# Performance work log

Measured on AMD Instinct MI355X. Metric: run time of the kernel, lower is better.

The kernel has to match this reference:

```python
import jax, jax.numpy as jnp
import numpy as np


def setup_inputs() -> dict:
    key = jax.random.key(0)
    k1, k2 = jax.random.split(key)
    n, d, ic, oc, r = 128, 256, 16, 16, 10
    x = jax.random.normal(k1, (n, d, ic, r), dtype=jnp.float32)
    weights = jax.random.normal(k2, (d, ic, oc, r), dtype=jnp.float32)
    return {"x": x, "weights": weights}


def reference(x, weights):
    # x: [n, d, ic, r]; weights: [d, ic, oc, r]
    # log_softmax over in_channels (dim=1 of weights)
    log_weights = jax.nn.log_softmax(weights, axis=1)  # [d, ic, oc, r]
    # broadcast add: x[n,d,ic,1,r] + lw[d,ic,oc,r] -> [n,d,ic,oc,r]
    z = x[:, :, :, None, :] + log_weights[None]
    # logsumexp over ic -> [n, d, oc, r]
    return jax.nn.logsumexp(z, axis=2)
```

## Files before the change

### kernel.cpp

```cpp
#include <hip/hip_runtime.h>
#include <hip/hip_bf16.h>


typedef __attribute__((ext_vector_type(8))) short bf16x8;
typedef __attribute__((ext_vector_type(4))) float f32x4;

__device__ __forceinline__ unsigned short f2bf(float v) {
    unsigned u = __float_as_uint(v);
    u += 0x7FFF + ((u >> 16) & 1);
    return (unsigned short)(u >> 16);
}

__global__ __launch_bounds__(256, 2) void fused_mfma_kernel(const float* __restrict__ x,
                                                            const float* __restrict__ w,
                                                            float* __restrict__ out) {
    __shared__ __align__(16) unsigned short es[64 * 328];
    __shared__ __align__(16) unsigned short ws_[10 * 640];
    __shared__ float lcs[160];

    const int tid = threadIdx.x;
    const int d   = blockIdx.x & 255;
    const int nb  = (blockIdx.x >> 8) << 6;

    {
        const int n_l = tid >> 2;
        const int seg = tid & 3;
        const float* xg = x + ((nb + n_l) * 256 + d) * 160 + seg * 40;
        float4 xv[10];
#pragma unroll
        for (int k = 0; k < 10; ++k) xv[k] = *reinterpret_cast<const float4*>(xg + 4 * k);

        const float* wgp = w + d * 2560 + tid * 10;
        float wv[10];
#pragma unroll
        for (int k = 0; k < 5; ++k) {
            float2 v = *reinterpret_cast<const float2*>(wgp + 2 * k);
            wv[2 * k] = v.x; wv[2 * k + 1] = v.y;
        }

        const float* xf = reinterpret_cast<const float*>(xv);
#pragma unroll
        for (int r = 0; r < 10; ++r) {
            unsigned short s0 = f2bf(__expf(xf[r]));
            unsigned short s1 = f2bf(__expf(xf[10 + r]));
            unsigned short s2 = f2bf(__expf(xf[20 + r]));
            unsigned short s3 = f2bf(__expf(xf[30 + r]));
            const unsigned lo = (unsigned)s0 | ((unsigned)s1 << 16);
            const unsigned hi = (unsigned)s2 | ((unsigned)s3 << 16);
            unsigned* dst = reinterpret_cast<unsigned*>(&es[n_l * 328 + r * 32 + 4 * seg]);
            *reinterpret_cast<uint2*>(dst) = make_uint2(lo, hi);
            unsigned* pad = reinterpret_cast<unsigned*>(&es[n_l * 328 + r * 32 + 16 + 4 * seg]);
            *reinterpret_cast<uint2*>(pad) = make_uint2(0u, 0u);
        }
#pragma unroll
        for (int k = 0; k < 10; ++k) {
            const int off = tid * 10 + k;
            const int ic  = off / 160;
            const int rem = off - ic * 160;
            const int oc  = rem / 10;
            const int r   = rem - oc * 10;
            ws_[r * 640 + oc * 40 + ic] = f2bf(__expf(wv[k]));
        }
        if (tid < 160) {
            const int r = tid >> 4, oc = tid & 15;
            uint4* p = reinterpret_cast<uint4*>(&ws_[r * 640 + oc * 40 + 16]);
            const uint4 z = make_uint4(0u, 0u, 0u, 0u);
            p[0] = z; p[1] = z;
        }
    }
    __syncthreads();

    if (tid < 160) {
        const int oc = tid / 10, r = tid - (tid / 10) * 10;
        const unsigned short* p = &ws_[r * 640 + oc * 40];
        float s = 0.f;
#pragma unroll
        for (int ic = 0; ic < 16; ++ic)
            s += __uint_as_float(((unsigned)p[ic]) << 16);
        lcs[oc * 10 + r] = __logf(s);
    }

    const int mt = tid >> 6;
    const int l  = tid & 63;
    const int lm = l & 15;
    const int kg = l >> 4;

    const int abase = (mt * 16 + lm) * 328 + kg * 8;
    const int bbase = lm * 40 + kg * 8;

    f32x4 acc[10];
    const f32x4 zero = {0.f, 0.f, 0.f, 0.f};
#pragma unroll
    for (int r = 0; r < 10; ++r) {
        bf16x8 a = *reinterpret_cast<const bf16x8*>(&es[abase + r * 32]);
        bf16x8 b = *reinterpret_cast<const bf16x8*>(&ws_[r * 640 + bbase]);
        acc[r] = __builtin_amdgcn_mfma_f32_16x16x32_bf16(a, b, zero, 0, 0, 0);
    }
    __syncthreads();

    float lc[10];
#pragma unroll
    for (int r = 0; r < 10; ++r) lc[r] = lcs[lm * 10 + r];

#pragma unroll
    for (int j = 0; j < 4; ++j) {
        const int n = mt * 16 + kg * 4 + j;
        float* og = out + ((nb + n) * 256 + d) * 160 + lm * 10;
#pragma unroll
        for (int h = 0; h < 5; ++h) {
            float2 o;
            o.x = __logf(acc[2 * h][j])     - lc[2 * h];
            o.y = __logf(acc[2 * h + 1][j]) - lc[2 * h + 1];
            *reinterpret_cast<float2*>(og + 2 * h) = o;
        }
    }
}

extern "C" void kernel_launch(void* const* d_in, const int* in_sizes, int n_in,
                              void* d_out, int out_size, void* d_ws, size_t ws_size,
                              hipStream_t stream) {
    const float* x = (const float*)d_in[0];
    const float* w = (const float*)d_in[1];
    float* out = (float*)d_out;

    fused_mfma_kernel<<<512, 256, 0, stream>>>(x, w, out);
}
```

Measured before the change: 16.52 us.

## Halve batch tile per block and split r across waves to double grid

```diff
diff --git a/kernel.cpp b/kernel.cpp
--- a/kernel.cpp
+++ b/kernel.cpp
@@ -11,59 +11,48 @@
     return (unsigned short)(u >> 16);
 }
 
-__global__ __launch_bounds__(256, 2) void fused_mfma_kernel(const float* __restrict__ x,
+__global__ __launch_bounds__(256, 4) void fused_mfma_kernel(const float* __restrict__ x,
                                                             const float* __restrict__ w,
                                                             float* __restrict__ out) {
-    __shared__ __align__(16) unsigned short es[64 * 328];
+    __shared__ __align__(16) unsigned short es[32 * 168];
     __shared__ __align__(16) unsigned short ws_[10 * 640];
     __shared__ float lcs[160];
 
     const int tid = threadIdx.x;
     const int d   = blockIdx.x & 255;
-    const int nb  = (blockIdx.x >> 8) << 6;
+    const int n_b = (blockIdx.x >> 8) << 5;
 
     {
-        const int n_l = tid >> 2;
-        const int seg = tid & 3;
-        const float* xg = x + ((nb + n_l) * 256 + d) * 160 + seg * 40;
-        float4 xv[10];
+        const int n_l  = tid >> 3;
+        const int part = tid & 7;
+        const float* xg = x + ((n_b + n_l) * 256 + d) * 160 + part * 20;
+        float4 xv[5];
 #pragma unroll
-        for (int k = 0; k < 10; ++k) xv[k] = *reinterpret_cast<const float4*>(xg + 4 * k);
+        for (int k = 0; k < 5; ++k) xv[k] = *reinterpret_cast<const float4*>(xg + 4 * k);
+        const float* xf = reinterpret_cast<const float*>(xv);
+        unsigned short* erow = &es[n_l * 168];
+#pragma unroll
+        for (int r = 0; r < 10; ++r) {
+            const unsigned v = (unsigned)f2bf(__expf(xf[r])) |
+                               ((unsigned)f2bf(__expf(xf[10 + r])) << 16);
+            *reinterpret_cast<unsigned*>(&erow[r * 16 + part * 2]) = v;
+        }
 
         const float* wgp = w + d * 2560 + tid * 10;
         float wv[10];
 #pragma unroll
         for (int k = 0; k < 5; ++k) {
-            float2 v = *reinterpret_cast<const float2*>(wgp + 2 * k);
-            wv[2 * k] = v.x; wv[2 * k + 1] = v.y;
+            float2 v2 = *reinterpret_cast<const float2*>(wgp + 2 * k);
+            wv[2 * k] = v2.x; wv[2 * k + 1] = v2.y;
         }
+        const int ic = tid >> 4, oc = tid & 15;
+#pragma unroll
+        for (int r = 0; r < 10; ++r)
+            ws_[r * 640 + oc * 40 + ic] = f2bf(__expf(wv[r]));
 
-        const float* xf = reinterpret_cast<const float*>(xv);
-#pragma unroll
-        for (int r = 0; r < 10; ++r) {
-            unsigned short s0 = f2bf(__expf(xf[r]));
-            unsigned short s1 = f2bf(__expf(xf[10 + r]));
-            unsigned short s2 = f2bf(__expf(xf[20 + r]));
-            unsigned short s3 = f2bf(__expf(xf[30 + r]));
-            const unsigned lo = (unsigned)s0 | ((unsigned)s1 << 16);
-            const unsigned hi = (unsigned)s2 | ((unsigned)s3 << 16);
-            unsigned* dst = reinterpret_cast<unsigned*>(&es[n_l * 328 + r * 32 + 4 * seg]);
-            *reinterpret_cast<uint2*>(dst) = make_uint2(lo, hi);
-            unsigned* pad = reinterpret_cast<unsigned*>(&es[n_l * 328 + r * 32 + 16 + 4 * seg]);
-            *reinterpret_cast<uint2*>(pad) = make_uint2(0u, 0u);
-        }
-#pragma unroll
-        for (int k = 0; k < 10; ++k) {
-            const int off = tid * 10 + k;
-            const int ic  = off / 160;
-            const int rem = off - ic * 160;
-            const int oc  = rem / 10;
-            const int r   = rem - oc * 10;
-            ws_[r * 640 + oc * 40 + ic] = f2bf(__expf(wv[k]));
-        }
         if (tid < 160) {
-            const int r = tid >> 4, oc = tid & 15;
-            uint4* p = reinterpret_cast<uint4*>(&ws_[r * 640 + oc * 40 + 16]);
+            const int r2 = tid >> 4, oc2 = tid & 15;
+            uint4* p = reinterpret_cast<uint4*>(&ws_[r2 * 640 + oc2 * 40 + 16]);
             const uint4 z = make_uint4(0u, 0u, 0u, 0u);
             p[0] = z; p[1] = z;
         }
@@ -71,47 +60,60 @@
     __syncthreads();
 
     if (tid < 160) {
-        const int oc = tid / 10, r = tid - (tid / 10) * 10;
+        const int r = tid >> 4, oc = tid & 15;
         const unsigned short* p = &ws_[r * 640 + oc * 40];
+        const uint4 q0 = *reinterpret_cast<const uint4*>(p);
+        const uint4 q1 = *reinterpret_cast<const uint4*>(p + 8);
+        const unsigned qs[8] = {q0.x, q0.y, q0.z, q0.w, q1.x, q1.y, q1.z, q1.w};
         float s = 0.f;
 #pragma unroll
-        for (int ic = 0; ic < 16; ++ic)
-            s += __uint_as_float(((unsigned)p[ic]) << 16);
+        for (int i = 0; i < 8; ++i) {
+            s += __uint_as_float(qs[i] << 16);
+            s += __uint_as_float(qs[i] & 0xFFFF0000u);
+        }
         lcs[oc * 10 + r] = __logf(s);
     }
 
-    const int mt = tid >> 6;
-    const int l  = tid & 63;
-    const int lm = l & 15;
-    const int kg = l >> 4;
+    const int wid = tid >> 6;
+    const int mt  = wid & 1;
+    const int rh  = wid >> 1;
+    const int l   = tid & 63;
+    const int lm  = l & 15;
+    const int kg  = l >> 4;
 
-    const int abase = (mt * 16 + lm) * 328 + kg * 8;
-    const int bbase = lm * 40 + kg * 8;
-
-    f32x4 acc[10];
-    const f32x4 zero = {0.f, 0.f, 0.f, 0.f};
+    const bf16x8 zero8 = {0, 0, 0, 0, 0, 0, 0, 0};
+    const f32x4  zeroc = {0.f, 0.f, 0.f, 0.f};
+    f32x4 acc[5];
 #pragma unroll
-    for (int r = 0; r < 10; ++r) {
-        bf16x8 a = *reinterpret_cast<const bf16x8*>(&es[abase + r * 32]);
-        bf16x8 b = *reinterpret_cast<const bf16x8*>(&ws_[r * 640 + bbase]);
-        acc[r] = __builtin_amdgcn_mfma_f32_16x16x32_bf16(a, b, zero, 0, 0, 0);
+    for (int h = 0; h < 5; ++h) {
+        const int r = rh * 5 + h;
+        bf16x8 a = (kg < 2)
+            ? *reinterpret_cast<const bf16x8*>(&es[(mt * 16 + lm) * 168 + r * 16 + kg * 8])
+            : zero8;
+        bf16x8 b = *reinterpret_cast<const bf16x8*>(&ws_[r * 640 + lm * 40 + kg * 8]);
+        acc[h] = __builtin_amdgcn_mfma_f32_16x16x32_bf16(a, b, zeroc, 0, 0, 0);
     }
     __syncthreads();
 
-    float lc[10];
+    float lc[5];
 #pragma unroll
-    for (int r = 0; r < 10; ++r) lc[r] = lcs[lm * 10 + r];
+    for (int h = 0; h < 5; ++h) lc[h] = lcs[lm * 10 + rh * 5 + h];
 
 #pragma unroll
     for (int j = 0; j < 4; ++j) {
-        const int n = mt * 16 + kg * 4 + j;
-        float* og = out + ((nb + n) * 256 + d) * 160 + lm * 10;
+        const int n = n_b + mt * 16 + kg * 4 + j;
+        float* og = out + (n * 256 + d) * 160 + lm * 10 + rh * 5;
+        float o[5];
 #pragma unroll
-        for (int h = 0; h < 5; ++h) {
-            float2 o;
-            o.x = __logf(acc[2 * h][j])     - lc[2 * h];
-            o.y = __logf(acc[2 * h + 1][j]) - lc[2 * h + 1];
-            *reinterpret_cast<float2*>(og + 2 * h) = o;
+        for (int h = 0; h < 5; ++h) o[h] = __logf(acc[h][j]) - lc[h];
+        if (rh == 0) {
+            *reinterpret_cast<float2*>(og)     = make_float2(o[0], o[1]);
+            *reinterpret_cast<float2*>(og + 2) = make_float2(o[2], o[3]);
+            og[4] = o[4];
+        } else {
+            og[0] = o[0];
+            *reinterpret_cast<float2*>(og + 1) = make_float2(o[1], o[2]);
+            *reinterpret_cast<float2*>(og + 3) = make_float2(o[3], o[4]);
         }
     }
 }
@@ -123,5 +125,5 @@
     const float* w = (const float*)d_in[1];
     float* out = (float*)d_out;
 
-    fused_mfma_kernel<<<512, 256, 0, stream>>>(x, w, out);
+    fused_mfma_kernel<<<1024, 256, 0, stream>>>(x, w, out);
 }
```

After: 16.72 us. About the same (+1.2%).
